# Performance work log

Measured on AMD Instinct MI355X. Metric: run time of the kernel, lower is better.

The kernel has to match this reference:

```python
import jax, jax.numpy as jnp
import numpy as np

DIM = 384
WS = 8        # window_size
SHIFT = 4     # shift_size
HEADS = 8
HEAD_DIM = DIM // HEADS
SCALE = HEAD_DIM ** (-0.5)
EPS = 1e-5


def layernorm(x, g, b):
    m = jnp.mean(x, axis=-1, keepdims=True)
    v = jnp.var(x, axis=-1, keepdims=True)
    return (x - m) * jax.lax.rsqrt(v + EPS) * g + b


def setup_inputs() -> dict:
    key = jax.random.key(0)
    ks = jax.random.split(key, 8)
    s = 0.02
    return {
        "x": jax.random.normal(ks[0], (8, DIM, 64, 64), dtype=jnp.float32),
        "qkv_w": jax.random.normal(ks[1], (DIM, 3 * DIM), dtype=jnp.float32) * s,
        "qkv_b": jnp.zeros((3 * DIM,), jnp.float32),
        "proj_w": jax.random.normal(ks[2], (DIM, DIM), dtype=jnp.float32) * s,
        "proj_b": jnp.zeros((DIM,), jnp.float32),
        "ln1_g": jnp.ones((DIM,), jnp.float32),
        "ln1_b": jnp.zeros((DIM,), jnp.float32),
        "ln2_g": jnp.ones((DIM,), jnp.float32),
        "ln2_b": jnp.zeros((DIM,), jnp.float32),
        "mlp_w1": jax.random.normal(ks[3], (DIM, 4 * DIM), dtype=jnp.float32) * s,
        "mlp_b1": jnp.zeros((4 * DIM,), jnp.float32),
        "mlp_w2": jax.random.normal(ks[4], (4 * DIM, DIM), dtype=jnp.float32) * s,
        "mlp_b2": jnp.zeros((DIM,), jnp.float32),
    }


def reference(x, qkv_w, qkv_b, proj_w, proj_b, ln1_g, ln1_b, ln2_g, ln2_b,
              mlp_w1, mlp_b1, mlp_w2, mlp_b2):
    B, C, H, W = x.shape
    x_skip = jnp.transpose(x, (0, 2, 3, 1))  # [B,H,W,C]
    xh = x_skip
    pad_b = (-H) % WS
    pad_r = (-W) % WS
    xh = jnp.pad(xh, ((0, 0), (0, pad_b), (0, pad_r), (0, 0)))
    Hp, Wp = xh.shape[1], xh.shape[2]
    if SHIFT > 0:
        xh = jnp.roll(xh, (-SHIFT, -SHIFT), axis=(1, 2))
    # window partition -> [B*nH*nW, WS*WS, C]
    win = xh.reshape(B, Hp // WS, WS, Wp // WS, WS, C)
    win = win.transpose(0, 1, 3, 2, 4, 5).reshape(-1, WS * WS, C)
    win = layernorm(win, ln1_g, ln1_b)
    # windowed MHA (no shift mask in original module)
    Bw, N, _ = win.shape
    qkv = (win @ qkv_w + qkv_b).reshape(Bw, N, 3, HEADS, HEAD_DIM)
    qkv = qkv.transpose(2, 0, 3, 1, 4)  # [3, Bw, H, N, d]
    q, k, v = qkv[0] * SCALE, qkv[1], qkv[2]
    attn = jax.nn.softmax(jnp.einsum('bhnd,bhmd->bhnm', q, k), axis=-1)
    out = jnp.einsum('bhnm,bhmd->bhnd', attn, v)
    out = out.transpose(0, 2, 1, 3).reshape(Bw, N, C)
    out = out @ proj_w + proj_b
    # window reverse
    xh = out.reshape(B, Hp // WS, Wp // WS, WS, WS, C)
    xh = xh.transpose(0, 1, 3, 2, 4, 5).reshape(B, Hp, Wp, C)
    if SHIFT > 0:
        xh = jnp.roll(xh, (SHIFT, SHIFT), axis=(1, 2))
    xh = xh[:, :H, :W, :] + x_skip
    h = layernorm(xh, ln2_g, ln2_b)
    h = jax.nn.gelu(h @ mlp_w1 + mlp_b1, approximate=False) @ mlp_w2 + mlp_b2
    return jnp.transpose(h, (0, 3, 1, 2))  # [B,C,H,W]
```

## Files before the change

### kernel.cpp

```cpp
#include <hip/hip_runtime.h>
#include <hip/hip_bf16.h>
#include <math.h>

#define DIM   384
#define HEADS 8
#define HD    48
#define NTOK  32768
#define NWIN  512

typedef __attribute__((ext_vector_type(8))) short bf16x8;
typedef __attribute__((ext_vector_type(8))) unsigned short u16x8;
typedef __attribute__((ext_vector_type(4))) float f32x4;

__device__ __forceinline__ float bf2f(unsigned short u) {
    unsigned int v = ((unsigned int)u) << 16;
    return __uint_as_float(v);
}
__device__ __forceinline__ unsigned short f2bf(float f) {
    unsigned int x = __float_as_uint(f);
    unsigned int r = (x + 0x7fffu + ((x >> 16) & 1u)) >> 16;
    return (unsigned short)r;
}

__device__ __forceinline__ float gelu(float v) {
    float z  = v * 0.70710678118654752f;
    float az = fabsf(z);
    float t  = __builtin_amdgcn_rcpf(1.0f + 0.47047f * az);
    float p  = t * (0.3480242f + t * (-0.0958798f + t * 0.7478556f));
    float ea = 1.0f - p * __expf(-az * az);
    float er = copysignf(ea, z);
    return 0.5f * v * (1.0f + er);
}

__device__ __forceinline__ void tok2src(int tok, int& b, int& hs, int& ws) {
    int bb  = tok >> 12;
    int win = (tok >> 6) & 63;
    int t   = tok & 63;
    int hi = win >> 3, wi = win & 7;
    int r  = t >> 3,  cc = t & 7;
    b  = bb;
    hs = (hi * 8 + r  + 4) & 63;
    ws = (wi * 8 + cc + 4) & 63;
}

__global__ __launch_bounds__(256) void k_wt4(const float* __restrict__ qkv_w,
                                             const float* __restrict__ proj_w,
                                             const float* __restrict__ w1,
                                             const float* __restrict__ w2,
                                             unsigned short* __restrict__ d0,
                                             unsigned short* __restrict__ d1,
                                             unsigned short* __restrict__ d2,
                                             unsigned short* __restrict__ d3) {
    int idx = blockIdx.x * 256 + threadIdx.x;
    const float* W; unsigned short* Wt; int K, N, loc;
    if (idx < 442368)       { W = qkv_w;  Wt = d0; K = 384;  N = 1152; loc = idx; }
    else if (idx < 589824)  { W = proj_w; Wt = d1; K = 384;  N = 384;  loc = idx - 442368; }
    else if (idx < 1179648) { W = w1;     Wt = d2; K = 384;  N = 1536; loc = idx - 589824; }
    else                    { W = w2;     Wt = d3; K = 1536; N = 384;  loc = idx - 1179648; }
    int n = loc / K, k = loc - n * K;
    Wt[loc] = f2bf(W[(size_t)k * N + n]);
}

__global__ __launch_bounds__(256) void k_ln1(const float* __restrict__ x,
                                             const float* __restrict__ g,
                                             const float* __restrict__ bt,
                                             unsigned short* __restrict__ ln1) {
    int blk = blockIdx.x;
    int b  = blk >> 6, hs = blk & 63;
    int t  = threadIdx.x;
    int w  = t & 63, cg = t >> 6;
    const float* row = x + (size_t)b * DIM * 4096 + hs * 64;

    float sum = 0.f, sq = 0.f;
    for (int i = 0; i < 96; i++) {
        int c = i * 4 + cg;
        float v = row[(size_t)c * 4096 + w];
        sum += v; sq += v * v;
    }
    __shared__ float red[2][4][64];
    __shared__ float mean_s[64], rstd_s[64];
    red[0][cg][w] = sum; red[1][cg][w] = sq;
    __syncthreads();
    if (t < 64) {
        float s  = red[0][0][t] + red[0][1][t] + red[0][2][t] + red[0][3][t];
        float q2 = red[1][0][t] + red[1][1][t] + red[1][2][t] + red[1][3][t];
        float mean = s * (1.0f / DIM);
        float var  = q2 * (1.0f / DIM) - mean * mean;
        mean_s[t] = mean;
        rstd_s[t] = rsqrtf(var + 1e-5f);
    }
    __syncthreads();

    int wp = t >> 2, seg = t & 3;
    int hr = (hs + 60) & 63, wr = (wp + 60) & 63;
    int tok = ((b * 8 + (hr >> 3)) * 8 + (wr >> 3)) * 64 + (hr & 7) * 8 + (wr & 7);

    __shared__ __align__(16) unsigned short tile[64][72];
    for (int chunk = 0; chunk < 6; chunk++) {
        float mean = mean_s[w], rstd = rstd_s[w];
        #pragma unroll
        for (int it = 0; it < 16; it++) {
            int cl = it * 4 + cg;
            int c  = chunk * 64 + cl;
            float v = row[(size_t)c * 4096 + w];
            tile[w][cl] = f2bf((v - mean) * rstd * g[c] + bt[c]);
        }
        __syncthreads();
        u16x8 v0 = *(const u16x8*)&tile[wp][seg * 16];
        u16x8 v1 = *(const u16x8*)&tile[wp][seg * 16 + 8];
        unsigned short* op = ln1 + (size_t)tok * DIM + chunk * 64 + seg * 16;
        *(u16x8*)op = v0;
        *(u16x8*)(op + 8) = v1;
        __syncthreads();
    }
}

template <int EPI>
__global__ __launch_bounds__(256) void k_gemm_mfma(
        const unsigned short* __restrict__ A,
        const unsigned short* __restrict__ Bt,
        const float* __restrict__ bias,
        void* __restrict__ Cout,
        const float* __restrict__ xres,
        int N, int K, int GX) {
    __shared__ __align__(16) unsigned short SH[24576];
    int tid  = threadIdx.x;
    int lane = tid & 63;
    int wave = tid >> 6;
    int wm = wave >> 1, wn = wave & 1;
    int quad = lane >> 4, l15 = lane & 15;

    int l   = blockIdx.x;
    int xcd = l & 7;
    int r_  = l >> 3;
    int bx  = r_ % GX;
    int by  = (r_ / GX) * 8 + xcd;
    int m0 = by * 128, n0 = bx * 128;

    const unsigned short* gA0 = A  + (size_t)(m0 +      lane) * K + wave * 8;
    const unsigned short* gA1 = A  + (size_t)(m0 + 64 + lane) * K + wave * 8;
    const unsigned short* gB0 = Bt + (size_t)(n0 +      lane) * K + wave * 8;
    const unsigned short* gB1 = Bt + (size_t)(n0 + 64 + lane) * K + wave * 8;

    auto stage = [&](int buf) {
        __builtin_amdgcn_global_load_lds(
            (const __attribute__((address_space(1))) void*)gA0,
            (__attribute__((address_space(3))) void*)&SH[buf * 4096 + wave * 1024],
            16, 0, 0);
        __builtin_amdgcn_global_load_lds(
            (const __attribute__((address_space(1))) void*)gA1,
            (__attribute__((address_space(3))) void*)&SH[buf * 4096 + wave * 1024 + 512],
            16, 0, 0);
        __builtin_amdgcn_global_load_lds(
            (const __attribute__((address_space(1))) void*)gB0,
            (__attribute__((address_space(3))) void*)&SH[12288 + buf * 4096 + wave * 1024],
            16, 0, 0);
        __builtin_amdgcn_global_load_lds(
            (const __attribute__((address_space(1))) void*)gB1,
            (__attribute__((address_space(3))) void*)&SH[12288 + buf * 4096 + wave * 1024 + 512],
            16, 0, 0);
        gA0 += 32; gA1 += 32; gB0 += 32; gB1 += 32;
    };

    f32x4 acc[4][4] = {};
    int nsteps = K >> 5;

    stage(0);
    stage(1);
    int cur = 0, nxt = 2;
    for (int t = 0; t < nsteps; ++t) {
        __builtin_amdgcn_s_barrier();
        if (t + 2 < nsteps) {
            stage(nxt);
            if (++nxt == 3) nxt = 0;
            asm volatile("s_waitcnt vmcnt(8)" ::: "memory");
        } else if (t + 2 == nsteps) {
            asm volatile("s_waitcnt vmcnt(4)" ::: "memory");
        } else {
            asm volatile("s_waitcnt vmcnt(0)" ::: "memory");
        }
        __builtin_amdgcn_s_barrier();

        bf16x8 af[4], bfr[4];
        #pragma unroll
        for (int r = 0; r < 4; r++)
            af[r] = *(const bf16x8*)&SH[cur * 4096 + (quad * 128 + wm * 64 + r * 16 + l15) * 8];
        #pragma unroll
        for (int r2 = 0; r2 < 4; r2++)
            bfr[r2] = *(const bf16x8*)&SH[12288 + cur * 4096 + (quad * 128 + wn * 64 + r2 * 16 + l15) * 8];
        #pragma unroll
        for (int r = 0; r < 4; r++)
            #pragma unroll
            for (int r2 = 0; r2 < 4; r2++)
                acc[r][r2] = __builtin_amdgcn_mfma_f32_16x16x32_bf16(
                                 af[r], bfr[r2], acc[r][r2], 0, 0, 0);
        if (++cur == 3) cur = 0;
    }

    if (EPI == 2 || EPI == 3) {
        #pragma unroll
        for (int r2 = 0; r2 < 4; r2++) {
            int n = n0 + wn * 64 + r2 * 16 + l15;
            float bn = bias[n];
            #pragma unroll
            for (int r = 0; r < 4; r++) {
                #pragma unroll
                for (int reg = 0; reg < 4; reg++) {
                    int m = m0 + wm * 64 + r * 16 + quad * 4 + reg;
                    float v = acc[r][r2][reg] + bn;
                    if (EPI == 2) {
                        int b, hs, ws_;
                        tok2src(m, b, hs, ws_);
                        v += xres[(((size_t)b * DIM + n) * 64 + hs) * 64 + ws_];
                    }
                    ((float*)Cout)[(size_t)m * N + n] = v;
                }
            }
        }
    } else {
        __syncthreads();
        #pragma unroll
        for (int r2 = 0; r2 < 4; r2++) {
            int col = wn * 64 + r2 * 16 + l15;
            float bn = bias[n0 + col];
            #pragma unroll
            for (int r = 0; r < 4; r++) {
                int row0 = wm * 64 + r * 16 + quad * 4;
                #pragma unroll
                for (int reg = 0; reg < 4; reg++) {
                    int row = row0 + reg;
                    float v = acc[r][r2][reg] + bn;
                    if (EPI == 1) v = gelu(v);
                    SH[(row * 136 + col) ^ (((row >> 3) & 1) << 4)] = f2bf(v);
                }
            }
        }
        __syncthreads();
        #pragma unroll
        for (int i = 0; i < 8; i++) {
            int chunk = tid + i * 256;
            int m = chunk >> 4, nc = chunk & 15;
            int idx = (m * 136 + nc * 8) ^ (((m >> 3) & 1) << 4);
            u16x8 v = *(const u16x8*)&SH[idx];
            if (EPI == 4) {
                int n = n0 + nc * 8;
                int qi  = n / 384;
                int rem = n - qi * 384;
                int hh  = rem / 48;
                int d   = rem - hh * 48;
                *(u16x8*)&((unsigned short*)Cout)[((size_t)(qi * 8 + hh) * NTOK + m0 + m) * 48 + d] = v;
            } else {
                *(u16x8*)&((unsigned short*)Cout)[(size_t)(m0 + m) * N + n0 + nc * 8] = v;
            }
        }
    }
}

__global__ __launch_bounds__(256) void k_attn_mfma(
        const unsigned short* __restrict__ qkvh,
        unsigned short* __restrict__ attn) {
    __shared__ __align__(16) unsigned short lds[4][8064];
    int tid  = threadIdx.x;
    int lane = tid & 63;
    int wave = tid >> 6;
    int quad = lane >> 4, l15 = lane & 15;
    int win  = blockIdx.x;
    int tok0 = win * 64;
    unsigned short* VT = &lds[wave][0];
    unsigned short* P  = &lds[wave][3456];
    const float scale = 0.14433756729740643f;

    for (int hi = 0; hi < 2; hi++) {
        int h = wave + hi * 4;
        const unsigned short* qb = qkvh + ((size_t)(0 * 8 + h) * NTOK + tok0) * 48;
        const unsigned short* kb = qkvh + ((size_t)(1 * 8 + h) * NTOK + tok0) * 48;
        const unsigned short* vb = qkvh + ((size_t)(2 * 8 + h) * NTOK + tok0) * 48;

        #pragma unroll
        for (int i = 0; i < 6; i++) {
            u16x8 v = *(const u16x8*)&vb[lane * 48 + i * 8];
            #pragma unroll
            for (int j = 0; j < 8; j++)
                VT[(i * 8 + j) * 72 + lane] = v[j];
        }

        bf16x8 kf[4][2];
        #pragma unroll
        for (int ni = 0; ni < 4; ni++) {
            kf[ni][0] = *(const bf16x8*)&kb[(ni * 16 + l15) * 48 + quad * 8];
            bf16x8 z = {};
            if (quad < 2)
                z = *(const bf16x8*)&kb[(ni * 16 + l15) * 48 + 32 + quad * 8];
            kf[ni][1] = z;
        }

        f32x4 sacc[4][4] = {};
        #pragma unroll
        for (int mi = 0; mi < 4; mi++) {
            bf16x8 qf0 = *(const bf16x8*)&qb[(mi * 16 + l15) * 48 + quad * 8];
            bf16x8 qf1 = {};
            if (quad < 2)
                qf1 = *(const bf16x8*)&qb[(mi * 16 + l15) * 48 + 32 + quad * 8];
            #pragma unroll
            for (int ni = 0; ni < 4; ni++) {
                sacc[mi][ni] = __builtin_amdgcn_mfma_f32_16x16x32_bf16(qf0, kf[ni][0], sacc[mi][ni], 0, 0, 0);
                sacc[mi][ni] = __builtin_amdgcn_mfma_f32_16x16x32_bf16(qf1, kf[ni][1], sacc[mi][ni], 0, 0, 0);
            }
        }

        #pragma unroll
        for (int mi = 0; mi < 4; mi++) {
            #pragma unroll
            for (int reg = 0; reg < 4; reg++) {
                float s0 = sacc[mi][0][reg] * scale;
                float s1 = sacc[mi][1][reg] * scale;
                float s2 = sacc[mi][2][reg] * scale;
                float s3 = sacc[mi][3][reg] * scale;
                float mx = fmaxf(fmaxf(s0, s1), fmaxf(s2, s3));
                #pragma unroll
                for (int off = 1; off < 16; off <<= 1)
                    mx = fmaxf(mx, __shfl_xor(mx, off));
                float e0 = __expf(s0 - mx);
                float e1 = __expf(s1 - mx);
                float e2 = __expf(s2 - mx);
                float e3 = __expf(s3 - mx);
                float sm = e0 + e1 + e2 + e3;
                #pragma unroll
                for (int off = 1; off < 16; off <<= 1)
                    sm += __shfl_xor(sm, off);
                float inv = 1.0f / sm;
                int row = mi * 16 + quad * 4 + reg;
                P[row * 72 +  0 + l15] = f2bf(e0 * inv);
                P[row * 72 + 16 + l15] = f2bf(e1 * inv);
                P[row * 72 + 32 + l15] = f2bf(e2 * inv);
                P[row * 72 + 48 + l15] = f2bf(e3 * inv);
            }
        }

        bf16x8 vf[3][2];
        #pragma unroll
        for (int ni = 0; ni < 3; ni++)
            #pragma unroll
            for (int kt = 0; kt < 2; kt++)
                vf[ni][kt] = *(const bf16x8*)&VT[(ni * 16 + l15) * 72 + kt * 32 + quad * 8];

        #pragma unroll
        for (int mi = 0; mi < 4; mi++) {
            bf16x8 pf0 = *(const bf16x8*)&P[(mi * 16 + l15) * 72 + quad * 8];
            bf16x8 pf1 = *(const bf16x8*)&P[(mi * 16 + l15) * 72 + 32 + quad * 8];
            f32x4 o[3] = {};
            #pragma unroll
            for (int ni = 0; ni < 3; ni++) {
                o[ni] = __builtin_amdgcn_mfma_f32_16x16x32_bf16(pf0, vf[ni][0], o[ni], 0, 0, 0);
                o[ni] = __builtin_amdgcn_mfma_f32_16x16x32_bf16(pf1, vf[ni][1], o[ni], 0, 0, 0);
            }
            #pragma unroll
            for (int ni = 0; ni < 3; ni++)
                #pragma unroll
                for (int reg = 0; reg < 4; reg++) {
                    int tok = tok0 + mi * 16 + quad * 4 + reg;
                    attn[(size_t)tok * DIM + h * HD + ni * 16 + l15] = f2bf(o[ni][reg]);
                }
        }
    }
}

__global__ __launch_bounds__(64) void k_ln2(const float* __restrict__ y,
                                            const float* __restrict__ g,
                                            const float* __restrict__ bt,
                                            unsigned short* __restrict__ out) {
    int tok = blockIdx.x;
    int t   = threadIdx.x;
    const float* row = y + (size_t)tok * DIM;
    float v[6];
    float sum = 0.f, sq = 0.f;
    #pragma unroll
    for (int i = 0; i < 6; i++) {
        v[i] = row[i * 64 + t];
        sum += v[i]; sq += v[i] * v[i];
    }
    #pragma unroll
    for (int o = 32; o > 0; o >>= 1) {
        sum += __shfl_xor(sum, o, 64);
        sq  += __shfl_xor(sq, o, 64);
    }
    float mean = sum * (1.0f / DIM);
    float var  = sq * (1.0f / DIM) - mean * mean;
    float rstd = rsqrtf(var + 1e-5f);
    unsigned short* orow = out + (size_t)tok * DIM;
    #pragma unroll
    for (int i = 0; i < 6; i++) {
        int c = i * 64 + t;
        orow[c] = f2bf((v[i] - mean) * rstd * g[c] + bt[c]);
    }
}

__global__ __launch_bounds__(256) void k_out(const float* __restrict__ hbuf,
                                             float* __restrict__ out) {
    int bh = blockIdx.x;
    int b = bh >> 6, h = bh & 63;
    int t = threadIdx.x;
    __shared__ float T[64][193];
    int hh = (h + 60) & 63;
    int hi = hh >> 3, r = hh & 7;
    for (int half = 0; half < 2; half++) {
        int c0 = half * 192;
        for (int idx = t; idx < 64 * 192; idx += 256) {
            int w = idx / 192;
            int c = idx - w * 192;
            int ww = (w + 60) & 63;
            int wi = ww >> 3, cc2 = ww & 7;
            int tok = ((b * 8 + hi) * 8 + wi) * 64 + r * 8 + cc2;
            T[w][c] = hbuf[(size_t)tok * DIM + c0 + c];
        }
        __syncthreads();
        for (int idx = t; idx < 64 * 192; idx += 256) {
            int cc = idx >> 6;
            int w  = idx & 63;
            out[(((size_t)b * DIM + c0 + cc) * 64 + h) * 64 + w] = T[w][cc];
        }
        __syncthreads();
    }
}

extern "C" void kernel_launch(void* const* d_in, const int* in_sizes, int n_in,
                              void* d_out, int out_size, void* d_ws, size_t ws_size,
                              hipStream_t stream) {
    const float* x      = (const float*)d_in[0];
    const float* qkv_w  = (const float*)d_in[1];
    const float* qkv_b  = (const float*)d_in[2];
    const float* proj_w = (const float*)d_in[3];
    const float* proj_b = (const float*)d_in[4];
    const float* ln1_g  = (const float*)d_in[5];
    const float* ln1_b  = (const float*)d_in[6];
    const float* ln2_g  = (const float*)d_in[7];
    const float* ln2_b  = (const float*)d_in[8];
    const float* w1     = (const float*)d_in[9];
    const float* b1     = (const float*)d_in[10];
    const float* w2     = (const float*)d_in[11];
    const float* b2     = (const float*)d_in[12];

    char* ws = (char*)d_ws;
    unsigned short* qkv_wt  = (unsigned short*)(ws + 0);
    unsigned short* proj_wt = (unsigned short*)(ws + 884736);
    unsigned short* w1t     = (unsigned short*)(ws + 1179648);
    unsigned short* w2t     = (unsigned short*)(ws + 2359296);
    unsigned short* ln1     = (unsigned short*)(ws + 4194304);
    unsigned short* qkv     = (unsigned short*)(ws + 29360128);
    unsigned short* attn    = (unsigned short*)(ws + 104857600);
    float*          y       = (float*)(ws + 130023424);
    unsigned short* ln2     = ln1;
    unsigned short* mid     = qkv;
    float*          hbuf    = y;

    k_wt4<<<6912, 256, 0, stream>>>(qkv_w, proj_w, w1, w2, qkv_wt, proj_wt, w1t, w2t);
    k_ln1<<<512, 256, 0, stream>>>(x, ln1_g, ln1_b, ln1);
    k_gemm_mfma<4><<<9 * 256, 256, 0, stream>>>(ln1, qkv_wt, qkv_b, qkv, nullptr, 1152, 384, 9);
    k_attn_mfma<<<NWIN, 256, 0, stream>>>(qkv, attn);
    k_gemm_mfma<2><<<3 * 256, 256, 0, stream>>>(attn, proj_wt, proj_b, y, x, 384, 384, 3);
    k_ln2<<<NTOK, 64, 0, stream>>>(y, ln2_g, ln2_b, ln2);
    k_gemm_mfma<1><<<12 * 256, 256, 0, stream>>>(ln2, w1t, b1, mid, nullptr, 1536, 384, 12);
    k_gemm_mfma<3><<<3 * 256, 256, 0, stream>>>(mid, w2t, b2, hbuf, nullptr, 384, 1536, 3);
    k_out<<<NWIN, 256, 0, stream>>>(hbuf, (float*)d_out);
}
```

Before: 492.0 us.

## Load GEMM fragments directly from global into registers, dropping LDS staging

The MFMA GEMM no longer stages A/B tiles through a triple-buffered LDS pipeline with barriers. Each wave loads its MFMA fragments straight from global memory into registers, double-buffered over K steps, and LDS shrinks to what the epilogue needs. This removes barriers and LDS traffic, but A rows are now fetched once per wave column and B rows once per wave row, so global/L2 traffic roughly doubles and the loads are strided 16-byte accesses. The loop steps K by two, which assumes K/32 is even; that holds for the K of 384 and 1536 used here.

```diff
diff --git a/kernel.cpp b/kernel.cpp
--- a/kernel.cpp
+++ b/kernel.cpp
@@ -123,7 +123,7 @@
         void* __restrict__ Cout,
         const float* __restrict__ xres,
         int N, int K, int GX) {
-    __shared__ __align__(16) unsigned short SH[24576];
+    __shared__ __align__(16) unsigned short SH[17408];
     int tid  = threadIdx.x;
     int lane = tid & 63;
     int wave = tid >> 6;
@@ -137,64 +137,69 @@
     int by  = (r_ / GX) * 8 + xcd;
     int m0 = by * 128, n0 = bx * 128;
 
-    const unsigned short* gA0 = A  + (size_t)(m0 +      lane) * K + wave * 8;
-    const unsigned short* gA1 = A  + (size_t)(m0 + 64 + lane) * K + wave * 8;
-    const unsigned short* gB0 = Bt + (size_t)(n0 +      lane) * K + wave * 8;
-    const unsigned short* gB1 = Bt + (size_t)(n0 + 64 + lane) * K + wave * 8;
-
-    auto stage = [&](int buf) {
-        __builtin_amdgcn_global_load_lds(
-            (const __attribute__((address_space(1))) void*)gA0,
-            (__attribute__((address_space(3))) void*)&SH[buf * 4096 + wave * 1024],
-            16, 0, 0);
-        __builtin_amdgcn_global_load_lds(
-            (const __attribute__((address_space(1))) void*)gA1,
-            (__attribute__((address_space(3))) void*)&SH[buf * 4096 + wave * 1024 + 512],
-            16, 0, 0);
-        __builtin_amdgcn_global_load_lds(
-            (const __attribute__((address_space(1))) void*)gB0,
-            (__attribute__((address_space(3))) void*)&SH[12288 + buf * 4096 + wave * 1024],
-            16, 0, 0);
-        __builtin_amdgcn_global_load_lds(
-            (const __attribute__((address_space(1))) void*)gB1,
-            (__attribute__((address_space(3))) void*)&SH[12288 + buf * 4096 + wave * 1024 + 512],
-            16, 0, 0);
-        gA0 += 32; gA1 += 32; gB0 += 32; gB1 += 32;
-    };
+    const unsigned short* pa0 = A  + (size_t)(m0 + wm * 64 +  0 + l15) * K + quad * 8;
+    const unsigned short* pa1 = A  + (size_t)(m0 + wm * 64 + 16 + l15) * K + quad * 8;
+    const unsigned short* pa2 = A  + (size_t)(m0 + wm * 64 + 32 + l15) * K + quad * 8;
+    const unsigned short* pa3 = A  + (size_t)(m0 + wm * 64 + 48 + l15) * K + quad * 8;
+    const unsigned short* pb0 = Bt + (size_t)(n0 + wn * 64 +  0 + l15) * K + quad * 8;
+    const unsigned short* pb1 = Bt + (size_t)(n0 + wn * 64 + 16 + l15) * K + quad * 8;
+    const unsigned short* pb2 = Bt + (size_t)(n0 + wn * 64 + 32 + l15) * K + quad * 8;
+    const unsigned short* pb3 = Bt + (size_t)(n0 + wn * 64 + 48 + l15) * K + quad * 8;
 
     f32x4 acc[4][4] = {};
     int nsteps = K >> 5;
 
-    stage(0);
-    stage(1);
-    int cur = 0, nxt = 2;
-    for (int t = 0; t < nsteps; ++t) {
-        __builtin_amdgcn_s_barrier();
-        if (t + 2 < nsteps) {
-            stage(nxt);
-            if (++nxt == 3) nxt = 0;
-            asm volatile("s_waitcnt vmcnt(8)" ::: "memory");
-        } else if (t + 2 == nsteps) {
-            asm volatile("s_waitcnt vmcnt(4)" ::: "memory");
-        } else {
-            asm volatile("s_waitcnt vmcnt(0)" ::: "memory");
-        }
-        __builtin_amdgcn_s_barrier();
-
-        bf16x8 af[4], bfr[4];
-        #pragma unroll
-        for (int r = 0; r < 4; r++)
-            af[r] = *(const bf16x8*)&SH[cur * 4096 + (quad * 128 + wm * 64 + r * 16 + l15) * 8];
-        #pragma unroll
-        for (int r2 = 0; r2 < 4; r2++)
-            bfr[r2] = *(const bf16x8*)&SH[12288 + cur * 4096 + (quad * 128 + wn * 64 + r2 * 16 + l15) * 8];
-        #pragma unroll
-        for (int r = 0; r < 4; r++)
-            #pragma unroll
-            for (int r2 = 0; r2 < 4; r2++)
-                acc[r][r2] = __builtin_amdgcn_mfma_f32_16x16x32_bf16(
-                                 af[r], bfr[r2], acc[r][r2], 0, 0, 0);
-        if (++cur == 3) cur = 0;
+    bf16x8 aX0 = *(const bf16x8*)pa0, aX1 = *(const bf16x8*)pa1;
+    bf16x8 aX2 = *(const bf16x8*)pa2, aX3 = *(const bf16x8*)pa3;
+    bf16x8 bX0 = *(const bf16x8*)pb0, bX1 = *(const bf16x8*)pb1;
+    bf16x8 bX2 = *(const bf16x8*)pb2, bX3 = *(const bf16x8*)pb3;
+
+    for (int t = 0; t < nsteps; t += 2) {
+        int o1 = (t + 1) << 5;
+        bf16x8 aY0 = *(const bf16x8*)(pa0 + o1), aY1 = *(const bf16x8*)(pa1 + o1);
+        bf16x8 aY2 = *(const bf16x8*)(pa2 + o1), aY3 = *(const bf16x8*)(pa3 + o1);
+        bf16x8 bY0 = *(const bf16x8*)(pb0 + o1), bY1 = *(const bf16x8*)(pb1 + o1);
+        bf16x8 bY2 = *(const bf16x8*)(pb2 + o1), bY3 = *(const bf16x8*)(pb3 + o1);
+
+        acc[0][0] = __builtin_amdgcn_mfma_f32_16x16x32_bf16(aX0, bX0, acc[0][0], 0, 0, 0);
+        acc[0][1] = __builtin_amdgcn_mfma_f32_16x16x32_bf16(aX0, bX1, acc[0][1], 0, 0, 0);
+        acc[0][2] = __builtin_amdgcn_mfma_f32_16x16x32_bf16(aX0, bX2, acc[0][2], 0, 0, 0);
+        acc[0][3] = __builtin_amdgcn_mfma_f32_16x16x32_bf16(aX0, bX3, acc[0][3], 0, 0, 0);
+        acc[1][0] = __builtin_amdgcn_mfma_f32_16x16x32_bf16(aX1, bX0, acc[1][0], 0, 0, 0);
+        acc[1][1] = __builtin_amdgcn_mfma_f32_16x16x32_bf16(aX1, bX1, acc[1][1], 0, 0, 0);
+        acc[1][2] = __builtin_amdgcn_mfma_f32_16x16x32_bf16(aX1, bX2, acc[1][2], 0, 0, 0);
+        acc[1][3] = __builtin_amdgcn_mfma_f32_16x16x32_bf16(aX1, bX3, acc[1][3], 0, 0, 0);
+        acc[2][0] = __builtin_amdgcn_mfma_f32_16x16x32_bf16(aX2, bX0, acc[2][0], 0, 0, 0);
+        acc[2][1] = __builtin_amdgcn_mfma_f32_16x16x32_bf16(aX2, bX1, acc[2][1], 0, 0, 0);
+        acc[2][2] = __builtin_amdgcn_mfma_f32_16x16x32_bf16(aX2, bX2, acc[2][2], 0, 0, 0);
+        acc[2][3] = __builtin_amdgcn_mfma_f32_16x16x32_bf16(aX2, bX3, acc[2][3], 0, 0, 0);
+        acc[3][0] = __builtin_amdgcn_mfma_f32_16x16x32_bf16(aX3, bX0, acc[3][0], 0, 0, 0);
+        acc[3][1] = __builtin_amdgcn_mfma_f32_16x16x32_bf16(aX3, bX1, acc[3][1], 0, 0, 0);
+        acc[3][2] = __builtin_amdgcn_mfma_f32_16x16x32_bf16(aX3, bX2, acc[3][2], 0, 0, 0);
+        acc[3][3] = __builtin_amdgcn_mfma_f32_16x16x32_bf16(aX3, bX3, acc[3][3], 0, 0, 0);
+
+        int o2 = (t + 2 < nsteps) ? (t + 2) << 5 : 0;
+        aX0 = *(const bf16x8*)(pa0 + o2); aX1 = *(const bf16x8*)(pa1 + o2);
+        aX2 = *(const bf16x8*)(pa2 + o2); aX3 = *(const bf16x8*)(pa3 + o2);
+        bX0 = *(const bf16x8*)(pb0 + o2); bX1 = *(const bf16x8*)(pb1 + o2);
+        bX2 = *(const bf16x8*)(pb2 + o2); bX3 = *(const bf16x8*)(pb3 + o2);
+
+        acc[0][0] = __builtin_amdgcn_mfma_f32_16x16x32_bf16(aY0, bY0, acc[0][0], 0, 0, 0);
+        acc[0][1] = __builtin_amdgcn_mfma_f32_16x16x32_bf16(aY0, bY1, acc[0][1], 0, 0, 0);
+        acc[0][2] = __builtin_amdgcn_mfma_f32_16x16x32_bf16(aY0, bY2, acc[0][2], 0, 0, 0);
+        acc[0][3] = __builtin_amdgcn_mfma_f32_16x16x32_bf16(aY0, bY3, acc[0][3], 0, 0, 0);
+        acc[1][0] = __builtin_amdgcn_mfma_f32_16x16x32_bf16(aY1, bY0, acc[1][0], 0, 0, 0);
+        acc[1][1] = __builtin_amdgcn_mfma_f32_16x16x32_bf16(aY1, bY1, acc[1][1], 0, 0, 0);
+        acc[1][2] = __builtin_amdgcn_mfma_f32_16x16x32_bf16(aY1, bY2, acc[1][2], 0, 0, 0);
+        acc[1][3] = __builtin_amdgcn_mfma_f32_16x16x32_bf16(aY1, bY3, acc[1][3], 0, 0, 0);
+        acc[2][0] = __builtin_amdgcn_mfma_f32_16x16x32_bf16(aY2, bY0, acc[2][0], 0, 0, 0);
+        acc[2][1] = __builtin_amdgcn_mfma_f32_16x16x32_bf16(aY2, bY1, acc[2][1], 0, 0, 0);
+        acc[2][2] = __builtin_amdgcn_mfma_f32_16x16x32_bf16(aY2, bY2, acc[2][2], 0, 0, 0);
+        acc[2][3] = __builtin_amdgcn_mfma_f32_16x16x32_bf16(aY2, bY3, acc[2][3], 0, 0, 0);
+        acc[3][0] = __builtin_amdgcn_mfma_f32_16x16x32_bf16(aY3, bY0, acc[3][0], 0, 0, 0);
+        acc[3][1] = __builtin_amdgcn_mfma_f32_16x16x32_bf16(aY3, bY1, acc[3][1], 0, 0, 0);
+        acc[3][2] = __builtin_amdgcn_mfma_f32_16x16x32_bf16(aY3, bY2, acc[3][2], 0, 0, 0);
+        acc[3][3] = __builtin_amdgcn_mfma_f32_16x16x32_bf16(aY3, bY3, acc[3][3], 0, 0, 0);
     }
 
     if (EPI == 2 || EPI == 3) {
@@ -218,7 +223,6 @@
             }
         }
     } else {
-        __syncthreads();
         #pragma unroll
         for (int r2 = 0; r2 < 4; r2++) {
             int col = wn * 64 + r2 * 16 + l15;
```

New measurement: 692.3 us. +40.7%, slower.

## Fuse output transpose into final GEMM epilogue and tile weight transpose

Applied to the files above, without the earlier changes.

The final MLP GEMM now writes directly to the NCHW output. Its epilogue stages each 64-token window tile in shared memory and stores vectorised rows with the inverse shift applied, so the separate k_out kernel and its hbuf round trip are gone. The weight transpose/convert kernel now uses 64x64 shared-memory tiles for coalesced reads and writes. f2bf uses the compiler's bf16 conversion instead of manual rounding. The new epilogue adds extra syncs and shared-memory staging per block.

```diff
diff --git a/kernel.cpp b/kernel.cpp
--- a/kernel.cpp
+++ b/kernel.cpp
@@ -17,9 +17,8 @@
     return __uint_as_float(v);
 }
 __device__ __forceinline__ unsigned short f2bf(float f) {
-    unsigned int x = __float_as_uint(f);
-    unsigned int r = (x + 0x7fffu + ((x >> 16) & 1u)) >> 16;
-    return (unsigned short)r;
+    __bf16 b = (__bf16)f;
+    return __builtin_bit_cast(unsigned short, b);
 }
 
 __device__ __forceinline__ float gelu(float v) {
@@ -51,14 +50,28 @@
                                              unsigned short* __restrict__ d1,
                                              unsigned short* __restrict__ d2,
                                              unsigned short* __restrict__ d3) {
-    int idx = blockIdx.x * 256 + threadIdx.x;
-    const float* W; unsigned short* Wt; int K, N, loc;
-    if (idx < 442368)       { W = qkv_w;  Wt = d0; K = 384;  N = 1152; loc = idx; }
-    else if (idx < 589824)  { W = proj_w; Wt = d1; K = 384;  N = 384;  loc = idx - 442368; }
-    else if (idx < 1179648) { W = w1;     Wt = d2; K = 384;  N = 1536; loc = idx - 589824; }
-    else                    { W = w2;     Wt = d3; K = 1536; N = 384;  loc = idx - 1179648; }
-    int n = loc / K, k = loc - n * K;
-    Wt[loc] = f2bf(W[(size_t)k * N + n]);
+    __shared__ unsigned short T[64][66];
+    int b = blockIdx.x;
+    const float* W; unsigned short* Wt; int K, N, lt;
+    if (b < 108)      { W = qkv_w;  Wt = d0; K = 384;  N = 1152; lt = b; }
+    else if (b < 144) { W = proj_w; Wt = d1; K = 384;  N = 384;  lt = b - 108; }
+    else if (b < 288) { W = w1;     Wt = d2; K = 384;  N = 1536; lt = b - 144; }
+    else              { W = w2;     Wt = d3; K = 1536; N = 384;  lt = b - 288; }
+    int tn = N >> 6;
+    int k0 = (lt / tn) << 6, n0 = (lt % tn) << 6;
+    int t  = threadIdx.x;
+    int cl = t & 63, rw = t >> 6;
+    #pragma unroll
+    for (int p = 0; p < 16; p++) {
+        int kk = p * 4 + rw;
+        T[cl][kk] = f2bf(W[(size_t)(k0 + kk) * N + n0 + cl]);
+    }
+    __syncthreads();
+    #pragma unroll
+    for (int p = 0; p < 16; p++) {
+        int nn = p * 4 + rw;
+        Wt[(size_t)(n0 + nn) * K + k0 + cl] = T[nn][cl];
+    }
 }
 
 __global__ __launch_bounds__(256) void k_ln1(const float* __restrict__ x,
@@ -217,6 +230,46 @@
                 }
             }
         }
+    } else if (EPI == 5) {
+        float* SF = (float*)SH;
+        __syncthreads();
+        int b    = m0 >> 12;
+        int win0 = m0 >> 6;
+        #pragma unroll
+        for (int h2 = 0; h2 < 2; h2++) {
+            if (wm == h2) {
+                #pragma unroll
+                for (int r2 = 0; r2 < 4; r2++) {
+                    int c = wn * 64 + r2 * 16 + l15;
+                    float bn = bias[n0 + c];
+                    #pragma unroll
+                    for (int r = 0; r < 4; r++) {
+                        f32x4 v4;
+                        #pragma unroll
+                        for (int reg = 0; reg < 4; reg++)
+                            v4[reg] = acc[r][r2][reg] + bn;
+                        *(f32x4*)&SF[c * 68 + r * 16 + quad * 4] = v4;
+                    }
+                }
+            }
+            __syncthreads();
+            int win = win0 + h2;
+            int wi = win & 7, hi = (win >> 3) & 7;
+            #pragma unroll
+            for (int i = 0; i < 4; i++) {
+                int id = tid + i * 256;
+                int c  = id >> 3, r = id & 7;
+                f32x4 v0 = *(const f32x4*)&SF[c * 68 + r * 8];
+                f32x4 v1 = *(const f32x4*)&SF[c * 68 + r * 8 + 4];
+                int hs  = (hi * 8 + r + 4) & 63;
+                int ws0 = wi * 8 + 4;
+                int ws1 = (wi * 8 + 8) & 63;
+                float* dst = (float*)Cout + ((size_t)(b * DIM + n0 + c) * 64 + hs) * 64;
+                *(f32x4*)&dst[ws0] = v0;
+                *(f32x4*)&dst[ws1] = v1;
+            }
+            __syncthreads();
+        }
     } else {
         __syncthreads();
         #pragma unroll
@@ -392,34 +445,6 @@
     for (int i = 0; i < 6; i++) {
         int c = i * 64 + t;
         orow[c] = f2bf((v[i] - mean) * rstd * g[c] + bt[c]);
-    }
-}
-
-__global__ __launch_bounds__(256) void k_out(const float* __restrict__ hbuf,
-                                             float* __restrict__ out) {
-    int bh = blockIdx.x;
-    int b = bh >> 6, h = bh & 63;
-    int t = threadIdx.x;
-    __shared__ float T[64][193];
-    int hh = (h + 60) & 63;
-    int hi = hh >> 3, r = hh & 7;
-    for (int half = 0; half < 2; half++) {
-        int c0 = half * 192;
-        for (int idx = t; idx < 64 * 192; idx += 256) {
-            int w = idx / 192;
-            int c = idx - w * 192;
-            int ww = (w + 60) & 63;
-            int wi = ww >> 3, cc2 = ww & 7;
-            int tok = ((b * 8 + hi) * 8 + wi) * 64 + r * 8 + cc2;
-            T[w][c] = hbuf[(size_t)tok * DIM + c0 + c];
-        }
-        __syncthreads();
-        for (int idx = t; idx < 64 * 192; idx += 256) {
-            int cc = idx >> 6;
-            int w  = idx & 63;
-            out[(((size_t)b * DIM + c0 + cc) * 64 + h) * 64 + w] = T[w][cc];
-        }
-        __syncthreads();
     }
 }
 
@@ -451,15 +476,13 @@
     float*          y       = (float*)(ws + 130023424);
     unsigned short* ln2     = ln1;
     unsigned short* mid     = qkv;
-    float*          hbuf    = y;
-
-    k_wt4<<<6912, 256, 0, stream>>>(qkv_w, proj_w, w1, w2, qkv_wt, proj_wt, w1t, w2t);
+
+    k_wt4<<<432, 256, 0, stream>>>(qkv_w, proj_w, w1, w2, qkv_wt, proj_wt, w1t, w2t);
     k_ln1<<<512, 256, 0, stream>>>(x, ln1_g, ln1_b, ln1);
     k_gemm_mfma<4><<<9 * 256, 256, 0, stream>>>(ln1, qkv_wt, qkv_b, qkv, nullptr, 1152, 384, 9);
     k_attn_mfma<<<NWIN, 256, 0, stream>>>(qkv, attn);
     k_gemm_mfma<2><<<3 * 256, 256, 0, stream>>>(attn, proj_wt, proj_b, y, x, 384, 384, 3);
     k_ln2<<<NTOK, 64, 0, stream>>>(y, ln2_g, ln2_b, ln2);
     k_gemm_mfma<1><<<12 * 256, 256, 0, stream>>>(ln2, w1t, b1, mid, nullptr, 1536, 384, 12);
-    k_gemm_mfma<3><<<3 * 256, 256, 0, stream>>>(mid, w2t, b2, hbuf, nullptr, 384, 1536, 3);
-    k_out<<<NWIN, 256, 0, stream>>>(hbuf, (float*)d_out);
-}
+    k_gemm_mfma<5><<<3 * 256, 256, 0, stream>>>(mid, w2t, b2, (float*)d_out, nullptr, 384, 1536, 3);
+}
```

Result: no change. 488.5 us (-0.7%).
